# Optimization experiments

Measured on AMD Instinct MI355X. Metric: run time of the kernel, lower is better.

The kernel has to match this reference:

```python
import jax, jax.numpy as jnp
import numpy as np

# dims: B batches, N points/batch, S sampled points/batch, M image-projected points/batch,
# V voxels, (H,Wd) range-image size, HID hidden size, NSC scales, NCLS classes
B, N, S, M, V, H, Wd, HID, NSC, NCLS = 2, 120000, 40000, 30000, 100000, 256, 1024, 128, 4, 20


def setup_inputs() -> dict:
    key = jax.random.key(0)
    ks = jax.random.split(key, 24)
    f = jnp.float32
    w = lambda k, shp: (0.02 * jax.random.normal(k, shp, f))
    rows = jax.random.randint(ks[10], (B, M), 0, H, jnp.int32)
    cols = jax.random.randint(ks[11], (B, M), 0, Wd, jnp.int32)
    return {
        "pts_feat_layers": jax.random.normal(ks[0], (NSC, V, HID), f),
        "pts_sample_feat": jax.random.normal(ks[1], (NSC, B * S, HID), f),
        "img_latent_full": jax.random.normal(ks[2], (B, HID, H, Wd), f),
        "img_feat_layers": jax.random.normal(ks[3], (NSC, B * M, HID), f),
        "leaner_W": w(ks[4], (NSC, HID, HID)), "leaner_b": jnp.zeros((NSC, HID), f),
        "fcs1_W": w(ks[5], (NSC, 2 * HID, HID)), "fcs1_b": jnp.zeros((NSC, HID), f),
        "fcs2_W": w(ks[6], (NSC, HID, HID)), "fcs2_b": jnp.zeros((NSC, HID), f),
        "cls_W1": w(ks[7], (NSC * HID, 128)), "cls_b1": jnp.zeros((128,), f),
        "cls_W2": w(ks[8], (128, NCLS)), "cls_b2": jnp.zeros((NCLS,), f),
        "points_img": jnp.stack([rows, cols], axis=-1),              # [B,M,2]
        "point2img_index": jax.random.randint(ks[12], (B, M), 0, N, jnp.int32),
        "sample_index": jax.random.randint(ks[13], (B, S), 0, N, jnp.int32),
        "coors_inv": jax.random.randint(ks[14], (B * N,), 0, V, jnp.int32),
    }


def reference(pts_feat_layers, pts_sample_feat, img_latent_full, img_feat_layers,
              leaner_W, leaner_b, fcs1_W, fcs1_b, fcs2_W, fcs2_b,
              cls_W1, cls_b1, cls_W2, cls_b2,
              points_img, point2img_index, sample_index, coors_inv):
    dt = img_latent_full.dtype
    img_hw = jnp.transpose(img_latent_full, (0, 2, 3, 1))  # [B,H,Wd,HID]
    bar = jnp.arange(B)[:, None]
    # gather image features at projected pixel coords: [B,M,HID]
    img_at_pts = img_hw[bar, points_img[:, :, 0], points_img[:, :, 1]]
    # scatter image features to per-point slots (pts_img_batch_new): [B,N,HID]
    pimg = jax.vmap(lambda idx, v: jnp.zeros((N, HID), dt).at[idx].set(v))(point2img_index, img_at_pts)

    fuse_feats, enc_feats = [], []
    for i in range(NSC):
        # p2img_mapping_spsample: output values depend only on sampled feats + image gather
        sf = pts_sample_feat[i].reshape(B, S, HID)
        sp = jax.vmap(lambda idx, v: jnp.zeros((N, HID), dt).at[idx].set(v))(sample_index, sf)
        sp = sp + pimg  # sample_point_feat == sample_point_feat_f  [B,N,HID]
        # scatter fused point features back into voxel features, then gather per point
        pts_feat = pts_feat_layers[i].at[coors_inv].set(sp.reshape(B * N, HID))
        pts_point = pts_feat[coors_inv].reshape(B, N, HID)
        # p2img_mapping: gather the image-projected points per batch  [B*M,HID]
        pts_g = jnp.take_along_axis(pts_point, point2img_index[:, :, None], axis=1).reshape(B * M, HID)
        fl = jax.nn.relu(pts_g @ leaner_W[i] + leaner_b[i])
        fc = jnp.concatenate([img_feat_layers[i], fl], axis=1) @ fcs1_W[i] + fcs1_b[i]
        fw = jax.nn.sigmoid(fc @ fcs2_W[i] + fcs2_b[i])
        fuse_feats.append(jax.nn.relu(fc * fw))
        enc_feats.append(sp.reshape(B * N, HID))

    seg = jnp.concatenate(fuse_feats, axis=1)                       # [B*M, NSC*HID]
    img_seg_logits = jax.nn.relu(seg @ cls_W1 + cls_b1) @ cls_W2 + cls_b2  # [B*M, NCLS]
    output_3d = jnp.concatenate(enc_feats, axis=1)                  # [B*N, NSC*HID]
    return img_seg_logits, output_3d
```

## Files before the change

### kernel.cpp

```cpp
#include <hip/hip_runtime.h>
#include <hip/hip_bf16.h>
#include <math.h>

#define B_    2
#define N_    120000
#define S_    40000
#define M_    30000
#define V_    100000
#define H_    256
#define WD_   1024
#define HID_  128
#define NSC_  4
#define NCLS_ 20
#define BM_   60000
#define BS_   80000
#define BN_   240000

typedef __attribute__((ext_vector_type(8))) short bfrag8;
typedef __attribute__((ext_vector_type(4))) float facc4;
typedef __attribute__((ext_vector_type(4))) unsigned short usvec4;

__device__ __forceinline__ unsigned short f2bf(float f){
  unsigned u = __builtin_bit_cast(unsigned, f);
  u += 0x7fffu + ((u >> 16) & 1u);
  return (unsigned short)(u >> 16);
}
__device__ __forceinline__ float bf2f(unsigned short s){
  return __builtin_bit_cast(float, ((unsigned)s) << 16);
}

__global__ __launch_bounds__(256) void k_winners(const int* __restrict__ p2i,
    const int* __restrict__ si, const int* __restrict__ ci,
    int* __restrict__ win_p, int* __restrict__ win_s, int* __restrict__ win_c){
  int t = blockIdx.x * 256 + threadIdx.x;
  if (t < BM_) atomicMax(&win_p[(t / M_) * N_ + p2i[t]], t);
  if (t < BS_) atomicMax(&win_s[(t / S_) * N_ + si[t]], t);
  if (t < BN_) atomicMax(&win_c[ci[t]], t);
}

__global__ __launch_bounds__(256) void k_gidx(const int* __restrict__ p2i,
    const int* __restrict__ ci, const int* __restrict__ win_c, int* __restrict__ gidx){
  int t = blockIdx.x * 256 + threadIdx.x;
  if (t >= BM_) return;
  int j = (t / M_) * N_ + p2i[t];
  gidx[t] = win_c[ci[j]];
}

__global__ __launch_bounds__(256) void k_imggather(const float* __restrict__ img,
    const int* __restrict__ ptsimg, unsigned short* __restrict__ iap){
  int t = blockIdx.x * 256 + threadIdx.x;
  int row = t >> 7, h = t & 127;
  int b = row / M_;
  int r = ptsimg[row * 2 + 0];
  int c = ptsimg[row * 2 + 1];
  iap[t] = f2bf(img[(((size_t)b * HID_ + h) * H_ + r) * WD_ + c]);
}

__global__ __launch_bounds__(256) void k_out3d(const float* __restrict__ samp,
    const int* __restrict__ win_s, const int* __restrict__ win_p,
    const unsigned short* __restrict__ iap, float* __restrict__ o3d){
  int t = blockIdx.x * 256 + threadIdx.x;
  int j = t >> 5, q = t & 31;
  int sj = win_s[j], pj = win_p[j];
  facc4 iv = {0.f, 0.f, 0.f, 0.f};
  if (pj >= 0){
    usvec4 u = __builtin_nontemporal_load((const usvec4*)(iap + (size_t)pj * HID_ + q * 4));
    iv.x = bf2f(u.x); iv.y = bf2f(u.y); iv.z = bf2f(u.z); iv.w = bf2f(u.w);
  }
  #pragma unroll
  for (int i = 0; i < NSC_; i++){
    facc4 v = iv;
    if (sj >= 0){
      facc4 s = __builtin_nontemporal_load((const facc4*)(samp + ((size_t)i * BS_ + sj) * HID_ + q * 4));
      v += s;
    }
    __builtin_nontemporal_store(v, (facc4*)(o3d + (size_t)j * (NSC_ * HID_) + i * HID_ + q * 4));
  }
}

__global__ __launch_bounds__(256) void k_prep(const float* __restrict__ lW,
    const float* __restrict__ f1W, const float* __restrict__ f2W,
    const float* __restrict__ c1W, const float* __restrict__ c2W,
    unsigned short* __restrict__ lwT, unsigned short* __restrict__ f1T,
    unsigned short* __restrict__ f2T, unsigned short* __restrict__ c1T,
    unsigned short* __restrict__ c2T){
  int t = blockIdx.x * 256 + threadIdx.x;
  if (t < 65536){
    int i = t >> 14, r = t & 16383, n = r >> 7, k = r & 127;
    lwT[i * 16384 + n * 128 + k] = f2bf(lW[i * 16384 + k * 128 + n]);
  } else if (t < 196608){
    int e = t - 65536;
    int i = e >> 15, r = e & 32767, n = r >> 8, k = r & 255;
    f1T[i * 32768 + n * 256 + k] = f2bf(f1W[i * 32768 + k * 128 + n]);
  } else if (t < 262144){
    int e = t - 196608;
    int i = e >> 14, r = e & 16383, n = r >> 7, k = r & 127;
    f2T[i * 16384 + n * 128 + k] = f2bf(f2W[i * 16384 + k * 128 + n]);
  } else if (t < 327680){
    int e = t - 262144;
    int n = e >> 9, k = e & 511;
    c1T[n * 512 + k] = f2bf(c1W[k * 128 + n]);
  } else if (t < 330240){
    int e = t - 327680;
    int n = e >> 7, k = e & 127;
    c2T[n * 128 + k] = f2bf(c2W[k * NCLS_ + n]);
  }
}

__global__ __launch_bounds__(256, 3) void k_scales(
    const float* __restrict__ o3d, const int* __restrict__ gidx,
    const float* __restrict__ imgf,
    const unsigned short* __restrict__ lwT, const float* __restrict__ lb,
    const unsigned short* __restrict__ f1T, const float* __restrict__ f1b,
    const unsigned short* __restrict__ f2T, const float* __restrict__ f2b,
    unsigned short* __restrict__ seg){
  __shared__ char lds[49152];
  char* actL = lds + 32768;
  const int i  = blockIdx.x & 3;
  const int rb = blockIdx.x >> 2;
  const int lane = threadIdx.x & 63, wv = threadIdx.x >> 6;
  const int rl = lane & 15, kg = lane >> 4;
  const int rowBase = rb * 64 + wv * 16;
  const int row = rowBase + rl;
  const bool rv = row < BM_;
  const int lr = wv * 16 + rl;

  {
    const char* src = (const char*)(lwT + (size_t)i * 16384);
    for (int c = threadIdx.x; c < 2048; c += 256){
      int byte = c << 4; int n = byte >> 8;
      *(bfrag8*)(lds + (byte ^ ((n & 7) << 4))) = *(const bfrag8*)(src + byte);
    }
  }
  bfrag8 afr[4];
  {
    const float* aA = o3d + (size_t)(rv ? gidx[row] : 0) * (NSC_ * HID_) + i * HID_;
    #pragma unroll
    for (int kc = 0; kc < 4; kc++){
      int k0 = kc * 32 + kg * 8;
      facc4 s0 = {0,0,0,0}, s1 = {0,0,0,0};
      if (rv){ s0 = *(const facc4*)(aA + k0); s1 = *(const facc4*)(aA + k0 + 4); }
      bfrag8 a;
      a[0]=(short)f2bf(s0.x); a[1]=(short)f2bf(s0.y); a[2]=(short)f2bf(s0.z); a[3]=(short)f2bf(s0.w);
      a[4]=(short)f2bf(s1.x); a[5]=(short)f2bf(s1.y); a[6]=(short)f2bf(s1.z); a[7]=(short)f2bf(s1.w);
      afr[kc] = a;
    }
  }
  __syncthreads();
  facc4 accL[8];
  #pragma unroll
  for (int ct = 0; ct < 8; ct++) accL[ct] = (facc4){0.f,0.f,0.f,0.f};
  #pragma unroll
  for (int kc = 0; kc < 4; kc++){
    int k0 = kc * 32 + kg * 8;
    #pragma unroll
    for (int ct = 0; ct < 8; ct++){
      int col = ct * 16 + rl;
      int byte = (col << 8) + (k0 << 1);
      bfrag8 b = *(const bfrag8*)(lds + (byte ^ ((col & 7) << 4)));
      accL[ct] = __builtin_amdgcn_mfma_f32_16x16x32_bf16(afr[kc], b, accL[ct], 0, 0, 0);
    }
  }
  __syncthreads();
  {
    const float* bias = lb + i * HID_;
    #pragma unroll
    for (int ct = 0; ct < 8; ct++){
      int col = ct * 16 + rl;
      float bv = bias[col];
      #pragma unroll
      for (int r = 0; r < 4; r++){
        int ar = wv * 16 + kg * 4 + r;
        float v = accL[ct][r] + bv; v = v > 0.f ? v : 0.f;
        int byte = ar * 256 + col * 2;
        *(unsigned short*)(actL + (byte ^ ((ar & 7) << 4))) = f2bf(v);
      }
    }
    const char* src = (const char*)(f1T + (size_t)i * 32768);
    for (int c = threadIdx.x; c < 2048; c += 256){
      int n = c >> 4, off = (c & 15) << 4;
      *(bfrag8*)(lds + ((n * 256 + off) ^ ((n & 7) << 4))) =
          *(const bfrag8*)(src + (size_t)n * 512 + off);
    }
  }
  __syncthreads();
  facc4 accF[8];
  #pragma unroll
  for (int ct = 0; ct < 8; ct++) accF[ct] = (facc4){0.f,0.f,0.f,0.f};
  {
    const float* a1 = imgf + ((size_t)i * BM_ + (rv ? row : 0)) * HID_;
    #pragma unroll
    for (int kc = 0; kc < 4; kc++){
      int kk = kc * 32 + kg * 8;
      bfrag8 a = (bfrag8){0,0,0,0,0,0,0,0};
      if (rv){
        facc4 s0 = *(const facc4*)(a1 + kk);
        facc4 s1 = *(const facc4*)(a1 + kk + 4);
        a[0]=(short)f2bf(s0.x); a[1]=(short)f2bf(s0.y); a[2]=(short)f2bf(s0.z); a[3]=(short)f2bf(s0.w);
        a[4]=(short)f2bf(s1.x); a[5]=(short)f2bf(s1.y); a[6]=(short)f2bf(s1.z); a[7]=(short)f2bf(s1.w);
      }
      #pragma unroll
      for (int ct = 0; ct < 8; ct++){
        int col = ct * 16 + rl;
        int byte = (col << 8) + (kk << 1);
        bfrag8 b = *(const bfrag8*)(lds + (byte ^ ((col & 7) << 4)));
        accF[ct] = __builtin_amdgcn_mfma_f32_16x16x32_bf16(a, b, accF[ct], 0, 0, 0);
      }
    }
  }
  __syncthreads();
  {
    const char* src = (const char*)(f1T + (size_t)i * 32768) + 256;
    for (int c = threadIdx.x; c < 2048; c += 256){
      int n = c >> 4, off = (c & 15) << 4;
      *(bfrag8*)(lds + ((n * 256 + off) ^ ((n & 7) << 4))) =
          *(const bfrag8*)(src + (size_t)n * 512 + off);
    }
  }
  __syncthreads();
  #pragma unroll
  for (int kc = 0; kc < 4; kc++){
    int kl = kc * 32 + kg * 8;
    int byteA = lr * 256 + kl * 2;
    bfrag8 a = *(const bfrag8*)(actL + (byteA ^ ((lr & 7) << 4)));
    #pragma unroll
    for (int ct = 0; ct < 8; ct++){
      int col = ct * 16 + rl;
      int byte = (col << 8) + (kl << 1);
      bfrag8 b = *(const bfrag8*)(lds + (byte ^ ((col & 7) << 4)));
      accF[ct] = __builtin_amdgcn_mfma_f32_16x16x32_bf16(a, b, accF[ct], 0, 0, 0);
    }
  }
  __syncthreads();
  {
    const float* bias = f1b + i * HID_;
    #pragma unroll
    for (int ct = 0; ct < 8; ct++){
      int col = ct * 16 + rl;
      float bv = bias[col];
      #pragma unroll
      for (int r = 0; r < 4; r++){
        int ar = wv * 16 + kg * 4 + r;
        float v = accF[ct][r] + bv;
        accF[ct][r] = v;
        int byte = ar * 256 + col * 2;
        *(unsigned short*)(actL + (byte ^ ((ar & 7) << 4))) = f2bf(v);
      }
    }
    const char* src = (const char*)(f2T + (size_t)i * 16384);
    for (int c = threadIdx.x; c < 2048; c += 256){
      int byte = c << 4; int n = byte >> 8;
      *(bfrag8*)(lds + (byte ^ ((n & 7) << 4))) = *(const bfrag8*)(src + byte);
    }
  }
  __syncthreads();
  facc4 accT[8];
  #pragma unroll
  for (int ct = 0; ct < 8; ct++) accT[ct] = (facc4){0.f,0.f,0.f,0.f};
  #pragma unroll
  for (int kc = 0; kc < 4; kc++){
    int kk = kc * 32 + kg * 8;
    int byteA = lr * 256 + kk * 2;
    bfrag8 a = *(const bfrag8*)(actL + (byteA ^ ((lr & 7) << 4)));
    #pragma unroll
    for (int ct = 0; ct < 8; ct++){
      int col = ct * 16 + rl;
      int byte = (col << 8) + (kk << 1);
      bfrag8 b = *(const bfrag8*)(lds + (byte ^ ((col & 7) << 4)));
      accT[ct] = __builtin_amdgcn_mfma_f32_16x16x32_bf16(a, b, accT[ct], 0, 0, 0);
    }
  }
  {
    const float* bias2 = f2b + i * HID_;
    #pragma unroll
    for (int ct = 0; ct < 8; ct++){
      int col = ct * 16 + rl;
      float bv2 = bias2[col];
      #pragma unroll
      for (int r = 0; r < 4; r++){
        int orow = rowBase + kg * 4 + r;
        if (orow < BM_){
          float tv = accT[ct][r] + bv2;
          float fw = 1.f / (1.f + expf(-tv));
          float u = accF[ct][r] * fw;
          u = u > 0.f ? u : 0.f;
          seg[(size_t)orow * (NSC_ * HID_) + i * HID_ + col] = f2bf(u);
        }
      }
    }
  }
}

__global__ __launch_bounds__(256, 3) void k_cls(const unsigned short* __restrict__ seg,
    const unsigned short* __restrict__ c1T, const float* __restrict__ c1b,
    const unsigned short* __restrict__ c2T, const float* __restrict__ c2b,
    float* __restrict__ logits){
  __shared__ char lds[49152];
  char* actL = lds + 32768;
  const int lane = threadIdx.x & 63, wv = threadIdx.x >> 6;
  const int rl = lane & 15, kg = lane >> 4;
  const int rowBase = blockIdx.x * 64 + wv * 16;
  const int row = rowBase + rl;
  const bool rv = row < BM_;
  const unsigned short* ar = seg + (size_t)(rv ? row : 0) * 512;
  facc4 acc[8];
  #pragma unroll
  for (int ct = 0; ct < 8; ct++) acc[ct] = (facc4){0.f,0.f,0.f,0.f};
  for (int ph = 0; ph < 4; ph++){
    if (ph) __syncthreads();
    for (int c = threadIdx.x; c < 2048; c += 256){
      int n = c >> 4, off = (c & 15) << 4;
      *(bfrag8*)(lds + ((n * 256 + off) ^ ((n & 7) << 4))) =
          *(const bfrag8*)((const char*)c1T + (size_t)n * 1024 + ph * 256 + off);
    }
    __syncthreads();
    #pragma unroll
    for (int kc = 0; kc < 4; kc++){
      int kl = kc * 32 + kg * 8;
      bfrag8 a = (bfrag8){0,0,0,0,0,0,0,0};
      if (rv) a = *(const bfrag8*)(ar + ph * 128 + kl);
      #pragma unroll
      for (int ct = 0; ct < 8; ct++){
        int col = ct * 16 + rl;
        int byte = (col << 8) + (kl << 1);
        bfrag8 b = *(const bfrag8*)(lds + (byte ^ ((col & 7) << 4)));
        acc[ct] = __builtin_amdgcn_mfma_f32_16x16x32_bf16(a, b, acc[ct], 0, 0, 0);
      }
    }
  }
  __syncthreads();
  #pragma unroll
  for (int ct = 0; ct < 8; ct++){
    int col = ct * 16 + rl;
    float bv = c1b[col];
    #pragma unroll
    for (int r = 0; r < 4; r++){
      int arr = wv * 16 + kg * 4 + r;
      float v = acc[ct][r] + bv; v = v > 0.f ? v : 0.f;
      int byte = arr * 256 + col * 2;
      *(unsigned short*)(actL + (byte ^ ((arr & 7) << 4))) = f2bf(v);
    }
  }
  for (int c = threadIdx.x; c < 320; c += 256)
    *(bfrag8*)(lds + (c << 4)) = *(const bfrag8*)((const char*)c2T + (c << 4));
  __syncthreads();
  {
    int t = threadIdx.x;
    int lrd = t >> 2, n0 = (t & 3) * 5;
    int orow = blockIdx.x * 64 + lrd;
    if (orow < BM_){
      float accD[5];
      #pragma unroll
      for (int q = 0; q < 5; q++) accD[q] = c2b[n0 + q];
      #pragma unroll
      for (int k8 = 0; k8 < 16; k8++){
        int byteA = lrd * 256 + (k8 << 4);
        bfrag8 hv = *(const bfrag8*)(actL + (byteA ^ ((lrd & 7) << 4)));
        #pragma unroll
        for (int q = 0; q < 5; q++){
          bfrag8 w8 = *(const bfrag8*)(lds + (n0 + q) * 256 + (k8 << 4));
          #pragma unroll
          for (int e = 0; e < 8; e++)
            accD[q] += bf2f((unsigned short)hv[e]) * bf2f((unsigned short)w8[e]);
        }
      }
      #pragma unroll
      for (int q = 0; q < 5; q++)
        logits[(size_t)orow * NCLS_ + n0 + q] = accD[q];
    }
  }
}

extern "C" void kernel_launch(void* const* d_in, const int* in_sizes, int n_in,
                              void* d_out, int out_size, void* d_ws, size_t ws_size,
                              hipStream_t stream){
  const float* samp = (const float*)d_in[1];
  const float* img  = (const float*)d_in[2];
  const float* imgf = (const float*)d_in[3];
  const float* lW   = (const float*)d_in[4];
  const float* lb   = (const float*)d_in[5];
  const float* f1W  = (const float*)d_in[6];
  const float* f1b  = (const float*)d_in[7];
  const float* f2W  = (const float*)d_in[8];
  const float* f2b  = (const float*)d_in[9];
  const float* c1W  = (const float*)d_in[10];
  const float* c1b  = (const float*)d_in[11];
  const float* c2W  = (const float*)d_in[12];
  const float* c2b  = (const float*)d_in[13];
  const int* ptsimg = (const int*)d_in[14];
  const int* p2i    = (const int*)d_in[15];
  const int* si     = (const int*)d_in[16];
  const int* ci     = (const int*)d_in[17];

  char* ws = (char*)d_ws;
  int*   win_p = (int*)(ws + 0);
  int*   win_s = (int*)(ws + 960000);
  int*   win_c = (int*)(ws + 1920000);
  int*   gidx  = (int*)(ws + 2320128);
  unsigned short* iap = (unsigned short*)(ws + 2560256);
  unsigned short* seg = (unsigned short*)(ws + 17920384);
  unsigned short* lwT = (unsigned short*)(ws + 79360512);
  unsigned short* f1T = lwT + 65536;
  unsigned short* f2T = f1T + 131072;
  unsigned short* c1T = f2T + 65536;
  unsigned short* c2T = c1T + 65536;

  float* logits = (float*)d_out;
  float* o3d    = (float*)d_out + (size_t)BM_ * NCLS_;

  (void)hipMemsetAsync(ws, 0xFF, 2320000, stream);
  k_winners  <<<938,   256, 0, stream>>>(p2i, si, ci, win_p, win_s, win_c);
  k_imggather<<<30000, 256, 0, stream>>>(img, ptsimg, iap);
  k_gidx     <<<235,   256, 0, stream>>>(p2i, ci, win_c, gidx);
  k_prep     <<<1290,  256, 0, stream>>>(lW, f1W, f2W, c1W, c2W, lwT, f1T, f2T, c1T, c2T);
  k_out3d    <<<30000, 256, 0, stream>>>(samp, win_s, win_p, iap, o3d);
  k_scales   <<<3752,  256, 0, stream>>>(o3d, gidx, imgf, lwT, lb, f1T, f1b, f2T, f2b, seg);
  k_cls      <<<938,   256, 0, stream>>>(seg, c1T, c1b, c2T, c2b, logits);
}
```

Measured before the change: 462.1 us.

## Merge front-end kernels and fuse out3d with scales, recomputing gathered activations

Folds the image gather, winner atomics and weight prep into a single front kernel, and runs the output-3D assembly and the per-scale MLP in one launch with block-index dispatch. The scale blocks now compute the gather index inline and rebuild their input rows from the sampled features and the image-at-point buffer, so they no longer read back o3d or need the gidx kernel. The aim is fewer launches and no dependency on o3d being written before the MLP reads it. In exchange, the MLP blocks issue extra indirect lookups and two gathers per row, and sharing one launch with the heavy out3d blocks may hurt occupancy for the LDS-heavy scale blocks.

```diff
diff --git a/kernel.cpp b/kernel.cpp
--- a/kernel.cpp
+++ b/kernel.cpp
@@ -16,6 +16,9 @@
 #define BS_   80000
 #define BN_   240000
 
+#define SCALE_BLKS 3752
+#define OUT3D_BLKS 30000
+
 typedef __attribute__((ext_vector_type(8))) short bfrag8;
 typedef __attribute__((ext_vector_type(4))) float facc4;
 typedef __attribute__((ext_vector_type(4))) unsigned short usvec4;
@@ -29,92 +32,91 @@
   return __builtin_bit_cast(float, ((unsigned)s) << 16);
 }
 
-__global__ __launch_bounds__(256) void k_winners(const int* __restrict__ p2i,
-    const int* __restrict__ si, const int* __restrict__ ci,
-    int* __restrict__ win_p, int* __restrict__ win_s, int* __restrict__ win_c){
-  int t = blockIdx.x * 256 + threadIdx.x;
-  if (t < BM_) atomicMax(&win_p[(t / M_) * N_ + p2i[t]], t);
-  if (t < BS_) atomicMax(&win_s[(t / S_) * N_ + si[t]], t);
-  if (t < BN_) atomicMax(&win_c[ci[t]], t);
-}
-
-__global__ __launch_bounds__(256) void k_gidx(const int* __restrict__ p2i,
-    const int* __restrict__ ci, const int* __restrict__ win_c, int* __restrict__ gidx){
-  int t = blockIdx.x * 256 + threadIdx.x;
-  if (t >= BM_) return;
-  int j = (t / M_) * N_ + p2i[t];
-  gidx[t] = win_c[ci[j]];
-}
-
-__global__ __launch_bounds__(256) void k_imggather(const float* __restrict__ img,
-    const int* __restrict__ ptsimg, unsigned short* __restrict__ iap){
-  int t = blockIdx.x * 256 + threadIdx.x;
-  int row = t >> 7, h = t & 127;
-  int b = row / M_;
-  int r = ptsimg[row * 2 + 0];
-  int c = ptsimg[row * 2 + 1];
-  iap[t] = f2bf(img[(((size_t)b * HID_ + h) * H_ + r) * WD_ + c]);
-}
-
-__global__ __launch_bounds__(256) void k_out3d(const float* __restrict__ samp,
-    const int* __restrict__ win_s, const int* __restrict__ win_p,
-    const unsigned short* __restrict__ iap, float* __restrict__ o3d){
-  int t = blockIdx.x * 256 + threadIdx.x;
-  int j = t >> 5, q = t & 31;
-  int sj = win_s[j], pj = win_p[j];
-  facc4 iv = {0.f, 0.f, 0.f, 0.f};
-  if (pj >= 0){
-    usvec4 u = __builtin_nontemporal_load((const usvec4*)(iap + (size_t)pj * HID_ + q * 4));
-    iv.x = bf2f(u.x); iv.y = bf2f(u.y); iv.z = bf2f(u.z); iv.w = bf2f(u.w);
-  }
-  #pragma unroll
-  for (int i = 0; i < NSC_; i++){
-    facc4 v = iv;
-    if (sj >= 0){
-      facc4 s = __builtin_nontemporal_load((const facc4*)(samp + ((size_t)i * BS_ + sj) * HID_ + q * 4));
-      v += s;
-    }
-    __builtin_nontemporal_store(v, (facc4*)(o3d + (size_t)j * (NSC_ * HID_) + i * HID_ + q * 4));
-  }
-}
-
-__global__ __launch_bounds__(256) void k_prep(const float* __restrict__ lW,
-    const float* __restrict__ f1W, const float* __restrict__ f2W,
-    const float* __restrict__ c1W, const float* __restrict__ c2W,
+__global__ __launch_bounds__(256) void k_front(
+    const float* __restrict__ img, const int* __restrict__ ptsimg,
+    unsigned short* __restrict__ iap,
+    const int* __restrict__ p2i, const int* __restrict__ si,
+    const int* __restrict__ ci,
+    int* __restrict__ win_p, int* __restrict__ win_s, int* __restrict__ win_c,
+    const float* __restrict__ lW, const float* __restrict__ f1W,
+    const float* __restrict__ f2W, const float* __restrict__ c1W,
+    const float* __restrict__ c2W,
     unsigned short* __restrict__ lwT, unsigned short* __restrict__ f1T,
     unsigned short* __restrict__ f2T, unsigned short* __restrict__ c1T,
     unsigned short* __restrict__ c2T){
-  int t = blockIdx.x * 256 + threadIdx.x;
-  if (t < 65536){
-    int i = t >> 14, r = t & 16383, n = r >> 7, k = r & 127;
-    lwT[i * 16384 + n * 128 + k] = f2bf(lW[i * 16384 + k * 128 + n]);
-  } else if (t < 196608){
-    int e = t - 65536;
-    int i = e >> 15, r = e & 32767, n = r >> 8, k = r & 255;
-    f1T[i * 32768 + n * 256 + k] = f2bf(f1W[i * 32768 + k * 128 + n]);
-  } else if (t < 262144){
-    int e = t - 196608;
-    int i = e >> 14, r = e & 16383, n = r >> 7, k = r & 127;
-    f2T[i * 16384 + n * 128 + k] = f2bf(f2W[i * 16384 + k * 128 + n]);
-  } else if (t < 327680){
-    int e = t - 262144;
-    int n = e >> 9, k = e & 511;
-    c1T[n * 512 + k] = f2bf(c1W[k * 128 + n]);
-  } else if (t < 330240){
-    int e = t - 327680;
-    int n = e >> 7, k = e & 127;
-    c2T[n * 128 + k] = f2bf(c2W[k * NCLS_ + n]);
-  }
-}
-
-__global__ __launch_bounds__(256, 3) void k_scales(
-    const float* __restrict__ o3d, const int* __restrict__ gidx,
-    const float* __restrict__ imgf,
+  int bid = blockIdx.x;
+  if (bid < 30000){
+    int t = bid * 256 + threadIdx.x;
+    int row = t >> 7, h = t & 127;
+    int b = row / M_;
+    int r = ptsimg[row * 2 + 0];
+    int c = ptsimg[row * 2 + 1];
+    iap[t] = f2bf(img[(((size_t)b * HID_ + h) * H_ + r) * WD_ + c]);
+    return;
+  }
+  if (bid < 30938){
+    int t = (bid - 30000) * 256 + threadIdx.x;
+    if (t < BM_) atomicMax(&win_p[(t / M_) * N_ + p2i[t]], t);
+    if (t < BS_) atomicMax(&win_s[(t / S_) * N_ + si[t]], t);
+    if (t < BN_) atomicMax(&win_c[ci[t]], t);
+    return;
+  }
+  {
+    int t = (bid - 30938) * 256 + threadIdx.x;
+    if (t < 65536){
+      int i = t >> 14, r = t & 16383, n = r >> 7, k = r & 127;
+      lwT[i * 16384 + n * 128 + k] = f2bf(lW[i * 16384 + k * 128 + n]);
+    } else if (t < 196608){
+      int e = t - 65536;
+      int i = e >> 15, r = e & 32767, n = r >> 8, k = r & 255;
+      f1T[i * 32768 + n * 256 + k] = f2bf(f1W[i * 32768 + k * 128 + n]);
+    } else if (t < 262144){
+      int e = t - 196608;
+      int i = e >> 14, r = e & 16383, n = r >> 7, k = r & 127;
+      f2T[i * 16384 + n * 128 + k] = f2bf(f2W[i * 16384 + k * 128 + n]);
+    } else if (t < 327680){
+      int e = t - 262144;
+      int n = e >> 9, k = e & 511;
+      c1T[n * 512 + k] = f2bf(c1W[k * 128 + n]);
+    } else if (t < 330240){
+      int e = t - 327680;
+      int n = e >> 7, k = e & 127;
+      c2T[n * 128 + k] = f2bf(c2W[k * NCLS_ + n]);
+    }
+    return;
+  }
+}
+
+__global__ __launch_bounds__(256, 3) void k_mega(
+    const float* __restrict__ samp, const unsigned short* __restrict__ iap,
+    const int* __restrict__ win_p, const int* __restrict__ win_s,
+    const int* __restrict__ win_c, const int* __restrict__ p2i,
+    const int* __restrict__ ci, const float* __restrict__ imgf,
     const unsigned short* __restrict__ lwT, const float* __restrict__ lb,
     const unsigned short* __restrict__ f1T, const float* __restrict__ f1b,
     const unsigned short* __restrict__ f2T, const float* __restrict__ f2b,
-    unsigned short* __restrict__ seg){
+    unsigned short* __restrict__ seg, float* __restrict__ o3d){
   __shared__ char lds[49152];
+  if (blockIdx.x >= SCALE_BLKS){
+    int t = (blockIdx.x - SCALE_BLKS) * 256 + threadIdx.x;
+    int j = t >> 5, q = t & 31;
+    int sj = win_s[j], pj = win_p[j];
+    facc4 iv = {0.f, 0.f, 0.f, 0.f};
+    if (pj >= 0){
+      usvec4 u = __builtin_nontemporal_load((const usvec4*)(iap + (size_t)pj * HID_ + q * 4));
+      iv.x = bf2f(u.x); iv.y = bf2f(u.y); iv.z = bf2f(u.z); iv.w = bf2f(u.w);
+    }
+    #pragma unroll
+    for (int i = 0; i < NSC_; i++){
+      facc4 v = iv;
+      if (sj >= 0){
+        facc4 s = __builtin_nontemporal_load((const facc4*)(samp + ((size_t)i * BS_ + sj) * HID_ + q * 4));
+        v += s;
+      }
+      __builtin_nontemporal_store(v, (facc4*)(o3d + (size_t)j * (NSC_ * HID_) + i * HID_ + q * 4));
+    }
+    return;
+  }
   char* actL = lds + 32768;
   const int i  = blockIdx.x & 3;
   const int rb = blockIdx.x >> 2;
@@ -134,15 +136,29 @@
   }
   bfrag8 afr[4];
   {
-    const float* aA = o3d + (size_t)(rv ? gidx[row] : 0) * (NSC_ * HID_) + i * HID_;
+    int g = 0;
+    if (rv){ int b = row >= M_; g = win_c[ci[b * N_ + p2i[row]]]; }
+    int sj = rv ? win_s[g] : -1;
+    int pj = rv ? win_p[g] : -1;
+    const float* sp = samp + ((size_t)i * BS_ + (sj < 0 ? 0 : sj)) * HID_;
+    const unsigned short* pp = iap + (size_t)(pj < 0 ? 0 : pj) * HID_;
     #pragma unroll
     for (int kc = 0; kc < 4; kc++){
       int k0 = kc * 32 + kg * 8;
       facc4 s0 = {0,0,0,0}, s1 = {0,0,0,0};
-      if (rv){ s0 = *(const facc4*)(aA + k0); s1 = *(const facc4*)(aA + k0 + 4); }
+      if (sj >= 0){ s0 = *(const facc4*)(sp + k0); s1 = *(const facc4*)(sp + k0 + 4); }
+      float g0=0,g1=0,g2=0,g3=0,g4=0,g5=0,g6=0,g7=0;
+      if (pj >= 0){
+        usvec4 u0 = *(const usvec4*)(pp + k0);
+        usvec4 u1 = *(const usvec4*)(pp + k0 + 4);
+        g0=bf2f(u0.x); g1=bf2f(u0.y); g2=bf2f(u0.z); g3=bf2f(u0.w);
+        g4=bf2f(u1.x); g5=bf2f(u1.y); g6=bf2f(u1.z); g7=bf2f(u1.w);
+      }
       bfrag8 a;
-      a[0]=(short)f2bf(s0.x); a[1]=(short)f2bf(s0.y); a[2]=(short)f2bf(s0.z); a[3]=(short)f2bf(s0.w);
-      a[4]=(short)f2bf(s1.x); a[5]=(short)f2bf(s1.y); a[6]=(short)f2bf(s1.z); a[7]=(short)f2bf(s1.w);
+      a[0]=(short)f2bf(s0.x+g0); a[1]=(short)f2bf(s0.y+g1);
+      a[2]=(short)f2bf(s0.z+g2); a[3]=(short)f2bf(s0.w+g3);
+      a[4]=(short)f2bf(s1.x+g4); a[5]=(short)f2bf(s1.y+g5);
+      a[6]=(short)f2bf(s1.z+g6); a[7]=(short)f2bf(s1.w+g7);
       afr[kc] = a;
     }
   }
@@ -396,10 +412,9 @@
   int*   win_p = (int*)(ws + 0);
   int*   win_s = (int*)(ws + 960000);
   int*   win_c = (int*)(ws + 1920000);
-  int*   gidx  = (int*)(ws + 2320128);
-  unsigned short* iap = (unsigned short*)(ws + 2560256);
-  unsigned short* seg = (unsigned short*)(ws + 17920384);
-  unsigned short* lwT = (unsigned short*)(ws + 79360512);
+  unsigned short* iap = (unsigned short*)(ws + 2320128);
+  unsigned short* seg = (unsigned short*)(ws + 17680384);
+  unsigned short* lwT = (unsigned short*)(ws + 79120512);
   unsigned short* f1T = lwT + 65536;
   unsigned short* f2T = f1T + 131072;
   unsigned short* c1T = f2T + 65536;
@@ -409,11 +424,12 @@
   float* o3d    = (float*)d_out + (size_t)BM_ * NCLS_;
 
   (void)hipMemsetAsync(ws, 0xFF, 2320000, stream);
-  k_winners  <<<938,   256, 0, stream>>>(p2i, si, ci, win_p, win_s, win_c);
-  k_imggather<<<30000, 256, 0, stream>>>(img, ptsimg, iap);
-  k_gidx     <<<235,   256, 0, stream>>>(p2i, ci, win_c, gidx);
-  k_prep     <<<1290,  256, 0, stream>>>(lW, f1W, f2W, c1W, c2W, lwT, f1T, f2T, c1T, c2T);
-  k_out3d    <<<30000, 256, 0, stream>>>(samp, win_s, win_p, iap, o3d);
-  k_scales   <<<3752,  256, 0, stream>>>(o3d, gidx, imgf, lwT, lb, f1T, f1b, f2T, f2b, seg);
-  k_cls      <<<938,   256, 0, stream>>>(seg, c1T, c1b, c2T, c2b, logits);
-}
+  k_front<<<32228, 256, 0, stream>>>(img, ptsimg, iap, p2i, si, ci,
+                                     win_p, win_s, win_c,
+                                     lW, f1W, f2W, c1W, c2W,
+                                     lwT, f1T, f2T, c1T, c2T);
+  k_mega <<<SCALE_BLKS + OUT3D_BLKS, 256, 0, stream>>>(samp, iap,
+                                     win_p, win_s, win_c, p2i, ci, imgf,
+                                     lwT, lb, f1T, f1b, f2T, f2b, seg, o3d);
+  k_cls  <<<938, 256, 0, stream>>>(seg, c1T, c1b, c2T, c2b, logits);
+}
```

After: 489.7 us. 1.06x slower.
